# Kernel tuning notes

Hardware: AMD Instinct MI355X
Metric: run time of the kernel (lower is better)

The kernel has to match this reference:

```python
import jax, jax.numpy as jnp
import numpy as np

D_MODEL = 1024
HEADS = 16
D_K = D_MODEL // HEADS
THETA = 10000.0


def _rope(x, pos):
    # x: [B, H, S, d_k]; pos: [S]
    half = D_K // 2
    inv_freq = 1.0 / (THETA ** (jnp.arange(0, D_K, 2, dtype=jnp.float32) / D_K))  # [half]
    ang = pos.astype(jnp.float32)[:, None] * inv_freq[None, :]  # [S, half]
    cos, sin = jnp.cos(ang), jnp.sin(ang)
    x1 = x[..., 0::2]  # even components
    x2 = x[..., 1::2]  # odd components
    o1 = x1 * cos - x2 * sin
    o2 = x1 * sin + x2 * cos
    # interleave back to original layout
    out = jnp.stack([o1, o2], axis=-1).reshape(x.shape)
    return out


def setup_inputs() -> dict:
    key = jax.random.key(0)
    ks = jax.random.split(key, 5)
    B, S = 4, 2048
    scale = 1.0 / np.sqrt(D_MODEL)
    return {
        "x": jax.random.normal(ks[0], (B, S, D_MODEL), dtype=jnp.float32),
        "Wq": jax.random.normal(ks[1], (D_MODEL, D_MODEL), dtype=jnp.float32) * scale,
        "Wk": jax.random.normal(ks[2], (D_MODEL, D_MODEL), dtype=jnp.float32) * scale,
        "Wv": jax.random.normal(ks[3], (D_MODEL, D_MODEL), dtype=jnp.float32) * scale,
        "Wo": jax.random.normal(ks[4], (D_MODEL, D_MODEL), dtype=jnp.float32) * scale,
    }


def reference(x, Wq, Wk, Wv, Wo):
    B, S, _ = x.shape
    # Linear weights are [out, in]; y = x @ W.T
    def proj(W):
        y = jnp.einsum('bsd,ed->bse', x, W)
        return y.reshape(B, S, HEADS, D_K).transpose(0, 2, 1, 3)  # [B,H,S,d_k]
    Q, K, V = proj(Wq), proj(Wk), proj(Wv)
    pos = jnp.arange(S, dtype=jnp.int32)
    Q = _rope(Q, pos)
    K = _rope(K, pos)
    scores = jnp.einsum('bhqd,bhkd->bhqk', Q, K) / jnp.sqrt(jnp.float32(D_K))
    causal = jnp.tril(jnp.ones((S, S), dtype=bool))
    scores = jnp.where(causal, scores, jnp.finfo(scores.dtype).min)
    attn = jax.nn.softmax(scores, axis=-1)
    mh = jnp.einsum('bhqk,bhkd->bhqd', attn, V)  # [B,H,S,d_v]
    mh = mh.transpose(0, 2, 1, 3).reshape(B, S, D_MODEL)
    return jnp.einsum('bsd,ed->bse', mh, Wo)
```

## Files before the change

### kernel.cpp

```cpp
#include <hip/hip_runtime.h>

typedef unsigned short u16;
typedef unsigned int   u32;
typedef __attribute__((ext_vector_type(8))) short s16x8;
typedef __attribute__((ext_vector_type(4))) float f32x4;
typedef __attribute__((ext_vector_type(16))) float f32x16;
typedef __attribute__((ext_vector_type(2))) int i32x2;

#define D_MODEL 1024
#define S_LEN   2048
#define BATCH   4
#define HEADS   16
#define DK      64
#define M_TOTAL (BATCH * S_LEN)

#define QSCALE 0.18033688011112042f
#define ROPE_L2 0.41524101186092029f

__device__ __forceinline__ u16 f2b(float f) {
  u32 u = __float_as_uint(f);
  u32 r = u + 0x7FFFu + ((u >> 16) & 1u);
  return (u16)(r >> 16);
}
__device__ __forceinline__ u32 packtrunc(float f0, float f1) {
  return (__float_as_uint(f0) >> 16) | (__float_as_uint(f1) & 0xFFFF0000u);
}
__device__ __forceinline__ u32 packrn(float f0, float f1) {
  return (u32)f2b(f0) | ((u32)f2b(f1) << 16);
}

extern "C" __device__ float __ocml_native_exp2_f32(float);
__device__ __forceinline__ float fexp2(float x) {
#if __has_builtin(__builtin_amdgcn_exp2f)
  return __builtin_amdgcn_exp2f(x);
#else
  return __ocml_native_exp2_f32(x);
#endif
}

template<int N> __device__ __forceinline__ void waitvm() {
  asm volatile("s_waitcnt vmcnt(%0)" :: "n"(N) : "memory");
}
template<int N> __device__ __forceinline__ void waitlgkm() {
  asm volatile("s_waitcnt lgkmcnt(%0)" :: "n"(N) : "memory");
}

template<int OFF> __device__ __forceinline__ s16x8 ldsr(unsigned a) {
  s16x8 r;
  asm volatile("ds_read_b128 %0, %1 offset:%2" : "=v"(r) : "v"(a), "n"(OFF));
  return r;
}

typedef const __attribute__((address_space(1))) unsigned int* gas_u32p;
typedef __attribute__((address_space(3))) unsigned int* las_u32p;
#define GLL16(gp, lp) __builtin_amdgcn_global_load_lds((gas_u32p)(gp), (las_u32p)(lp), 16, 0, 0)

__global__ void k_cvt(const float* __restrict__ x,
                      const float* __restrict__ a, const float* __restrict__ b,
                      const float* __restrict__ c, const float* __restrict__ d,
                      u16* __restrict__ Xb, u16* __restrict__ Wb) {
  int i = blockIdx.x * blockDim.x + threadIdx.x;
  if (i < 2097152) {
    float4 v = ((const float4*)x)[i];
    ((u32*)Xb)[2 * i]     = packrn(v.x, v.y);
    ((u32*)Xb)[2 * i + 1] = packrn(v.z, v.w);
  } else {
    int j = i - 2097152;
    const float* src = (j < 524288) ? ((j < 262144) ? a : b) : ((j < 786432) ? c : d);
    float4 v = ((const float4*)src)[j & 0x3FFFF];
    ((u32*)Wb)[2 * j]     = packrn(v.x, v.y);
    ((u32*)Wb)[2 * j + 1] = packrn(v.z, v.w);
  }
}

template<bool BF16OUT, bool ROPE, bool DUAL>
__device__ __forceinline__ void gemm_body(u16* __restrict__ SH,
                                          const u16* __restrict__ A, const u16* __restrict__ B,
                                          void* __restrict__ C, void* __restrict__ C2,
                                          int bm, int bn, int N, int K, float scale) {
  constexpr int SLOT = 8192;
  const int tid  = threadIdx.x;
  const int lane = tid & 63;
  const int w    = tid >> 6;
  const int wm2  = w >> 1, wn2 = w & 1;
  const int rl   = lane & 15, q = lane >> 4;

  const int rowS = tid >> 2;
  const int blkS = (tid & 3) ^ ((lane >> 3) & 3);
  const u16* Asrc = A + (size_t)(bm + rowS) * K + blkS * 8;
  const u16* Bsrc = B + (size_t)(bn + rowS) * K + blkS * 8;

  const unsigned shb = (unsigned)(size_t)(las_u32p)SH;
  const int fbase = rl * 32 + ((q ^ ((rl >> 1) & 3)) * 8);
  const unsigned aR0 = shb + 2 * (wm2 * 2048 + fbase);
  const unsigned bR0 = shb + 2 * (4096 + wn2 * 2048 + fbase);

  f32x4 acc[4][4];
#pragma unroll
  for (int i = 0; i < 4; i++)
#pragma unroll
    for (int j = 0; j < 4; j++) acc[i][j] = (f32x4){0.f, 0.f, 0.f, 0.f};

  const int nt = K >> 5;

  auto stage = [&](int t) {
    const int k0 = t << 5;
    u16* d = SH + (t & 1) * SLOT + w * 512;
    GLL16(Asrc + k0, d);
    GLL16(Asrc + (size_t)64 * K + k0, d + 2048);
    GLL16(Bsrc + k0, d + 4096);
    GLL16(Bsrc + (size_t)64 * K + k0, d + 6144);
  };

  stage(0);

  for (int t = 0; t < nt; t++) {
    waitvm<0>();
    __builtin_amdgcn_s_barrier();

    const unsigned off = (unsigned)((t & 1) * (2 * SLOT));
    const unsigned aR = aR0 + off, bR = bR0 + off;
    s16x8 bf0 = ldsr<0>(bR),    bf1 = ldsr<1024>(bR);
    s16x8 bf2 = ldsr<2048>(bR), bf3 = ldsr<3072>(bR);
    s16x8 af0 = ldsr<0>(aR),    af1 = ldsr<1024>(aR);
    s16x8 af2 = ldsr<2048>(aR), af3 = ldsr<3072>(aR);

    if (t + 1 < nt) stage(t + 1);

    waitlgkm<3>();
    __builtin_amdgcn_sched_barrier(0);
    __builtin_amdgcn_s_setprio(1);
    acc[0][0] = __builtin_amdgcn_mfma_f32_16x16x32_bf16(af0, bf0, acc[0][0], 0, 0, 0);
    acc[0][1] = __builtin_amdgcn_mfma_f32_16x16x32_bf16(af0, bf1, acc[0][1], 0, 0, 0);
    acc[0][2] = __builtin_amdgcn_mfma_f32_16x16x32_bf16(af0, bf2, acc[0][2], 0, 0, 0);
    acc[0][3] = __builtin_amdgcn_mfma_f32_16x16x32_bf16(af0, bf3, acc[0][3], 0, 0, 0);
    waitlgkm<2>();
    __builtin_amdgcn_sched_barrier(0);
    acc[1][0] = __builtin_amdgcn_mfma_f32_16x16x32_bf16(af1, bf0, acc[1][0], 0, 0, 0);
    acc[1][1] = __builtin_amdgcn_mfma_f32_16x16x32_bf16(af1, bf1, acc[1][1], 0, 0, 0);
    acc[1][2] = __builtin_amdgcn_mfma_f32_16x16x32_bf16(af1, bf2, acc[1][2], 0, 0, 0);
    acc[1][3] = __builtin_amdgcn_mfma_f32_16x16x32_bf16(af1, bf3, acc[1][3], 0, 0, 0);
    waitlgkm<1>();
    __builtin_amdgcn_sched_barrier(0);
    acc[2][0] = __builtin_amdgcn_mfma_f32_16x16x32_bf16(af2, bf0, acc[2][0], 0, 0, 0);
    acc[2][1] = __builtin_amdgcn_mfma_f32_16x16x32_bf16(af2, bf1, acc[2][1], 0, 0, 0);
    acc[2][2] = __builtin_amdgcn_mfma_f32_16x16x32_bf16(af2, bf2, acc[2][2], 0, 0, 0);
    acc[2][3] = __builtin_amdgcn_mfma_f32_16x16x32_bf16(af2, bf3, acc[2][3], 0, 0, 0);
    waitlgkm<0>();
    __builtin_amdgcn_sched_barrier(0);
    acc[3][0] = __builtin_amdgcn_mfma_f32_16x16x32_bf16(af3, bf0, acc[3][0], 0, 0, 0);
    acc[3][1] = __builtin_amdgcn_mfma_f32_16x16x32_bf16(af3, bf1, acc[3][1], 0, 0, 0);
    acc[3][2] = __builtin_amdgcn_mfma_f32_16x16x32_bf16(af3, bf2, acc[3][2], 0, 0, 0);
    acc[3][3] = __builtin_amdgcn_mfma_f32_16x16x32_bf16(af3, bf3, acc[3][3], 0, 0, 0);
    __builtin_amdgcn_s_setprio(0);
  }

  const bool isQ = !DUAL || (bn < D_MODEL);
  u16* Cd = (u16*)(isQ ? C : C2);
  const int bnL = DUAL ? (bn & (D_MODEL - 1)) : bn;
  const float sc = isQ ? scale : 1.0f;

#pragma unroll
  for (int mi = 0; mi < 4; mi++)
#pragma unroll
    for (int ni = 0; ni < 4; ni++) {
      if (ROPE) {
        const int col = bnL + wn2 * 64 + ni * 16 + rl;
        const int fi  = (col & 63) >> 1;
        const float inv = exp2f(-(float)fi * ROPE_L2);
        const bool odd = (rl & 1);
#pragma unroll
        for (int r = 0; r < 4; r++) {
          int grow = bm + wm2 * 64 + mi * 16 + q * 4 + r;
          float own = acc[mi][ni][r];
          float oth = __shfl_xor(own, 1);
          float ang = (float)(grow & (S_LEN - 1)) * inv;
          float sn, cs;
          __sincosf(ang, &sn, &cs);
          float x1 = odd ? oth : own;
          float x2 = odd ? own : oth;
          float res = odd ? (x1 * sn + x2 * cs) : (x1 * cs - x2 * sn);
          acc[mi][ni][r] = res * sc;
        }
      }
#pragma unroll
      for (int r = 0; r < 4; r++) {
        int grow = bm + wm2 * 64 + mi * 16 + q * 4 + r;
        int gcol = bnL + wn2 * 64 + ni * 16 + rl;
        float v = acc[mi][ni][r];
        if (BF16OUT) Cd[(size_t)grow * N + gcol] = f2b(v);
        else         ((float*)Cd)[(size_t)grow * N + gcol] = v;
      }
    }
}

__launch_bounds__(256, 4)
__global__ void k_qkv(const u16* __restrict__ Xb, const u16* __restrict__ Wqkb,
                      const u16* __restrict__ Wvb,
                      u16* __restrict__ Qb, u16* __restrict__ Kb, u16* __restrict__ Vtg) {
  __shared__ u16 SH[16384];
  const int swz = (blockIdx.x & 7) * 192 + (blockIdx.x >> 3);
  if (swz < 1024) {
    gemm_body<true, true, true>(SH, Xb, Wqkb, Qb, Kb,
                                (swz >> 4) * 128, (swz & 15) * 128,
                                D_MODEL, D_MODEL, QSCALE);
  } else {
    const int b2 = swz - 1024;
    gemm_body<true, false, false>(SH, Wvb, Xb, Vtg, Vtg,
                                  (b2 >> 6) * 128, (b2 & 63) * 128,
                                  M_TOTAL, D_MODEL, 1.0f);
  }
}

__launch_bounds__(256, 4)
__global__ void k_out(const u16* __restrict__ Mh, const u16* __restrict__ Wob,
                      float* __restrict__ out) {
  __shared__ u16 SH[16384];
  const int swz = (blockIdx.x & 7) * 64 + (blockIdx.x >> 3);
  gemm_body<false, false, false>(SH, Mh, Wob, out, out,
                                 (swz >> 3) * 128, (swz & 7) * 128,
                                 D_MODEL, D_MODEL, 1.0f);
}

__launch_bounds__(256, 4)
__global__ void k_attn(const u16* __restrict__ Qb, const u16* __restrict__ Kb,
                       const u16* __restrict__ Vtg, u16* __restrict__ Mh) {
  __shared__ u16 SH[128 * 64 + 64 * 128];
  u16* Kl = SH;
  u16* Vt = SH + 128 * 64;
  const int tid  = threadIdx.x;
  const int lane = tid & 63;
  const int w    = tid >> 6;
  const int n    = lane & 31;
  const int h    = lane >> 5;
  const int nx   = n & 7;
  const int bid = blockIdx.x;
  const int r   = bid >> 3;
  const int u   = r & 15;
  const int bh  = (bid & 7) + 8 * (r >> 4);
  const int hd  = bh & 15, b = bh >> 4;
  const int s   = (w & 2) ? (62 - 2 * u + (w & 1)) : (2 * u + (w & 1));
  const int rb  = s * 32;
  const int ktiles = ((63 - 2 * u) >> 2) + 1;
  const size_t kbase = ((size_t)b * S_LEN) * D_MODEL + (size_t)hd * DK;
  const size_t vbase = ((size_t)hd * DK) * M_TOTAL + (size_t)b * S_LEN;

  const int hx    = ((h ^ nx) << 3);
  const int kidx0 = n * 64  + hx;
  const int vidx0 = n * 128 + hx;

  s16x8 bq[4];
#pragma unroll
  for (int ks = 0; ks < 4; ks++)
    bq[ks] = *(const s16x8*)(Qb + kbase + (size_t)(rb + n) * D_MODEL + ks * 16 + h * 8);

  f32x16 o[2];
#pragma unroll
  for (int dt = 0; dt < 2; dt++)
#pragma unroll
    for (int i = 0; i < 16; i++) o[dt][i] = 0.f;
  float psum = 0.f;

  const int krow_l = lane >> 3;
  const int kblk_l = (lane & 7) ^ krow_l;
  const u16* KgL = Kb + kbase + (size_t)(w * 32 + krow_l) * D_MODEL + kblk_l * 8;
  u16* KdL = Kl + (w * 32) * 64;
  const int vrow_l = lane >> 4;
  const int vblk_l = lane & 15;
  const u16* VgL = Vtg + vbase + (size_t)(w * 16 + vrow_l) * M_TOTAL;
  u16* VdL = Vt + (w * 16) * 128;

  for (int t = 0; t < ktiles; t++) {
    const int k0 = t * 128;
    __syncthreads();
#pragma unroll
    for (int i = 0; i < 4; i++)
      GLL16(KgL + (size_t)(k0 + i * 8) * D_MODEL, KdL + i * 8 * 64);
#pragma unroll
    for (int i = 0; i < 4; i++) {
      const int jj = vblk_l ^ ((i * 4 + vrow_l) & 7);
      GLL16(VgL + (size_t)(i * 4) * M_TOTAL + k0 + jj * 8, VdL + i * 4 * 128);
    }
    __syncthreads();

#pragma unroll
    for (int kt = 0; kt < 4; kt++) {
      const int k0t = k0 + kt * 32;
      if (k0t > rb + 31) continue;

      s16x8 ak[4], vf[4];
#pragma unroll
      for (int ks = 0; ks < 4; ks++)
        ak[ks] = *(const s16x8*)(Kl + ((kidx0 ^ (ks << 4)) + kt * 2048));
#pragma unroll
      for (int c = 0; c < 2; c++)
#pragma unroll
        for (int dt = 0; dt < 2; dt++)
          vf[c * 2 + dt] = *(const s16x8*)(Vt + ((vidx0 ^ (kt * 32 + c * 16)) + dt * 4096));

      f32x16 Sc;
#pragma unroll
      for (int i = 0; i < 16; i++) Sc[i] = 0.f;
#pragma unroll
      for (int ks = 0; ks < 4; ks++)
        Sc = __builtin_amdgcn_mfma_f32_32x32x16_bf16(ak[ks], bq[ks], Sc, 0, 0, 0);

      u32 P0[4], P1[4];
      float ps01 = 0.f, ps23 = 0.f;
      if ((k0t + 31) > rb) {
        const int lim = rb + n - k0t - 4 * h;
#pragma unroll
        for (int g = 0; g < 4; g++) {
          float pv[4];
#pragma unroll
          for (int t2 = 0; t2 < 4; t2++) {
            float e = fexp2(Sc[4 * g + t2]);
            pv[t2] = (8 * g + t2 <= lim) ? e : 0.f;
          }
          ps01 += pv[0] + pv[1];
          ps23 += pv[2] + pv[3];
          P0[g] = packtrunc(pv[0], pv[1]);
          P1[g] = packtrunc(pv[2], pv[3]);
        }
      } else {
#pragma unroll
        for (int g = 0; g < 4; g++) {
          float pv[4];
#pragma unroll
          for (int t2 = 0; t2 < 4; t2++) pv[t2] = fexp2(Sc[4 * g + t2]);
          ps01 += pv[0] + pv[1];
          ps23 += pv[2] + pv[3];
          P0[g] = packtrunc(pv[0], pv[1]);
          P1[g] = packtrunc(pv[2], pv[3]);
        }
      }
      psum += ps01 + ps23;

#pragma unroll
      for (int c = 0; c < 2; c++) {
        i32x2 rA = __builtin_amdgcn_permlane32_swap((int)P0[2 * c], (int)P0[2 * c + 1], false, false);
        i32x2 rB = __builtin_amdgcn_permlane32_swap((int)P1[2 * c], (int)P1[2 * c + 1], false, false);
        union { u32 uu[4]; s16x8 v; } pb;
        pb.uu[0] = (u32)rA[0];
        pb.uu[1] = (u32)rB[0];
        pb.uu[2] = (u32)rA[1];
        pb.uu[3] = (u32)rB[1];
        o[0] = __builtin_amdgcn_mfma_f32_32x32x16_bf16(vf[c * 2 + 0], pb.v, o[0], 0, 0, 0);
        o[1] = __builtin_amdgcn_mfma_f32_32x32x16_bf16(vf[c * 2 + 1], pb.v, o[1], 0, 0, 0);
      }
    }
  }

  float l = psum + __shfl_xor(psum, 32);
  const float linv = 1.0f / l;
  __syncthreads();
  u16* Olw = SH + w * 32 * 66;
#pragma unroll
  for (int dt = 0; dt < 2; dt++) {
#pragma unroll
    for (int g = 0; g < 4; g++) {
      u32 lo = packrn(o[dt][4 * g + 0] * linv, o[dt][4 * g + 1] * linv);
      u32 hi = packrn(o[dt][4 * g + 2] * linv, o[dt][4 * g + 3] * linv);
      *(uint2*)(Olw + n * 66 + dt * 32 + 8 * g + 4 * h) = (uint2){lo, hi};
    }
  }
  const int rr = lane >> 3, seg = lane & 7;
#pragma unroll
  for (int ro = 0; ro < 32; ro += 8) {
    uint4 v = *(const uint4*)(Olw + (ro + rr) * 66 + seg * 8);
    *(uint4*)(Mh + ((size_t)b * S_LEN + rb + ro + rr) * D_MODEL + hd * DK + seg * 8) = v;
  }
}

extern "C" void kernel_launch(void* const* d_in, const int* in_sizes, int n_in,
                              void* d_out, int out_size, void* d_ws, size_t ws_size,
                              hipStream_t stream) {
  const float* x  = (const float*)d_in[0];
  const float* Wq = (const float*)d_in[1];
  const float* Wk = (const float*)d_in[2];
  const float* Wv = (const float*)d_in[3];
  const float* Wo = (const float*)d_in[4];
  float* out = (float*)d_out;

  char* ws = (char*)d_ws;
  const size_t xsz = (size_t)M_TOTAL * D_MODEL * 2;
  const size_t wsz = (size_t)D_MODEL * D_MODEL * 2;
  u16* Xb  = (u16*)ws; ws += xsz;
  u16* Wqb = (u16*)ws; ws += wsz;
  u16* Wkb = (u16*)ws; ws += wsz;
  u16* Wvb = (u16*)ws; ws += wsz;
  u16* Wob = (u16*)ws; ws += wsz;
  u16* Qb  = (u16*)ws; ws += xsz;
  u16* Kb  = (u16*)ws; ws += xsz;
  u16* Vtg = (u16*)ws; ws += xsz;
  u16* Mh  = (u16*)ws; ws += xsz;

  k_cvt<<<12288, 256, 0, stream>>>(x, Wq, Wk, Wv, Wo, Xb, Wqb);

  k_qkv<<<1536, 256, 0, stream>>>(Xb, Wqb, Wvb, Qb, Kb, Vtg);

  k_attn<<<dim3(1024), 256, 0, stream>>>(Qb, Kb, Vtg, Mh);

  k_out<<<512, 256, 0, stream>>>(Mh, Wob, out);
}
```

Measured before the change: 245.2 us.

## Load K and V fragments directly from global memory in attention kernel

Removes the shared-memory staging of K and V tiles and the block-wide barriers; each wave now reads its K and V MFMA fragments straight from global memory (relying on L1/L2) and iterates only over its own causal key tiles. This drops LDS traffic and synchronisation and lets each wave stop at its own diagonal, but it loses cross-wave reuse of the loaded tiles and issues strided, less coalesced global loads with no prefetch overlap.

New measurement: 308.6 us. 1.26x slower.

```diff
diff --git a/kernel.cpp b/kernel.cpp
--- a/kernel.cpp
+++ b/kernel.cpp
@@ -225,15 +225,12 @@
 __launch_bounds__(256, 4)
 __global__ void k_attn(const u16* __restrict__ Qb, const u16* __restrict__ Kb,
                        const u16* __restrict__ Vtg, u16* __restrict__ Mh) {
-  __shared__ u16 SH[128 * 64 + 64 * 128];
-  u16* Kl = SH;
-  u16* Vt = SH + 128 * 64;
+  __shared__ u16 SH[4 * 32 * 66];
   const int tid  = threadIdx.x;
   const int lane = tid & 63;
   const int w    = tid >> 6;
   const int n    = lane & 31;
   const int h    = lane >> 5;
-  const int nx   = n & 7;
   const int bid = blockIdx.x;
   const int r   = bid >> 3;
   const int u   = r & 15;
@@ -241,19 +238,17 @@
   const int hd  = bh & 15, b = bh >> 4;
   const int s   = (w & 2) ? (62 - 2 * u + (w & 1)) : (2 * u + (w & 1));
   const int rb  = s * 32;
-  const int ktiles = ((63 - 2 * u) >> 2) + 1;
   const size_t kbase = ((size_t)b * S_LEN) * D_MODEL + (size_t)hd * DK;
   const size_t vbase = ((size_t)hd * DK) * M_TOTAL + (size_t)b * S_LEN;
 
-  const int hx    = ((h ^ nx) << 3);
-  const int kidx0 = n * 64  + hx;
-  const int vidx0 = n * 128 + hx;
-
   s16x8 bq[4];
 #pragma unroll
   for (int ks = 0; ks < 4; ks++)
     bq[ks] = *(const s16x8*)(Qb + kbase + (size_t)(rb + n) * D_MODEL + ks * 16 + h * 8);
 
+  const u16* KgL = Kb + kbase + (size_t)n * D_MODEL + h * 8;
+  const u16* VgL = Vtg + vbase + (size_t)n * M_TOTAL + h * 8;
+
   f32x16 o[2];
 #pragma unroll
   for (int dt = 0; dt < 2; dt++)
@@ -261,99 +256,73 @@
     for (int i = 0; i < 16; i++) o[dt][i] = 0.f;
   float psum = 0.f;
 
-  const int krow_l = lane >> 3;
-  const int kblk_l = (lane & 7) ^ krow_l;
-  const u16* KgL = Kb + kbase + (size_t)(w * 32 + krow_l) * D_MODEL + kblk_l * 8;
-  u16* KdL = Kl + (w * 32) * 64;
-  const int vrow_l = lane >> 4;
-  const int vblk_l = lane & 15;
-  const u16* VgL = Vtg + vbase + (size_t)(w * 16 + vrow_l) * M_TOTAL;
-  u16* VdL = Vt + (w * 16) * 128;
-
-  for (int t = 0; t < ktiles; t++) {
-    const int k0 = t * 128;
-    __syncthreads();
-#pragma unroll
-    for (int i = 0; i < 4; i++)
-      GLL16(KgL + (size_t)(k0 + i * 8) * D_MODEL, KdL + i * 8 * 64);
-#pragma unroll
-    for (int i = 0; i < 4; i++) {
-      const int jj = vblk_l ^ ((i * 4 + vrow_l) & 7);
-      GLL16(VgL + (size_t)(i * 4) * M_TOTAL + k0 + jj * 8, VdL + i * 4 * 128);
-    }
-    __syncthreads();
-
-#pragma unroll
-    for (int kt = 0; kt < 4; kt++) {
-      const int k0t = k0 + kt * 32;
-      if (k0t > rb + 31) continue;
-
-      s16x8 ak[4], vf[4];
-#pragma unroll
-      for (int ks = 0; ks < 4; ks++)
-        ak[ks] = *(const s16x8*)(Kl + ((kidx0 ^ (ks << 4)) + kt * 2048));
-#pragma unroll
-      for (int c = 0; c < 2; c++)
-#pragma unroll
-        for (int dt = 0; dt < 2; dt++)
-          vf[c * 2 + dt] = *(const s16x8*)(Vt + ((vidx0 ^ (kt * 32 + c * 16)) + dt * 4096));
-
-      f32x16 Sc;
-#pragma unroll
-      for (int i = 0; i < 16; i++) Sc[i] = 0.f;
-#pragma unroll
-      for (int ks = 0; ks < 4; ks++)
-        Sc = __builtin_amdgcn_mfma_f32_32x32x16_bf16(ak[ks], bq[ks], Sc, 0, 0, 0);
-
-      u32 P0[4], P1[4];
-      float ps01 = 0.f, ps23 = 0.f;
-      if ((k0t + 31) > rb) {
-        const int lim = rb + n - k0t - 4 * h;
-#pragma unroll
-        for (int g = 0; g < 4; g++) {
-          float pv[4];
-#pragma unroll
-          for (int t2 = 0; t2 < 4; t2++) {
-            float e = fexp2(Sc[4 * g + t2]);
-            pv[t2] = (8 * g + t2 <= lim) ? e : 0.f;
-          }
-          ps01 += pv[0] + pv[1];
-          ps23 += pv[2] + pv[3];
-          P0[g] = packtrunc(pv[0], pv[1]);
-          P1[g] = packtrunc(pv[2], pv[3]);
+  for (int st = 0; st <= s; st++) {
+    const int k0t = st * 32;
+
+    s16x8 ak[4], vf[4];
+#pragma unroll
+    for (int ks = 0; ks < 4; ks++)
+      ak[ks] = *(const s16x8*)(KgL + (size_t)k0t * D_MODEL + ks * 16);
+#pragma unroll
+    for (int c = 0; c < 2; c++)
+#pragma unroll
+      for (int dt = 0; dt < 2; dt++)
+        vf[c * 2 + dt] = *(const s16x8*)(VgL + (size_t)(dt * 32) * M_TOTAL + k0t + c * 16);
+
+    f32x16 Sc;
+#pragma unroll
+    for (int i = 0; i < 16; i++) Sc[i] = 0.f;
+#pragma unroll
+    for (int ks = 0; ks < 4; ks++)
+      Sc = __builtin_amdgcn_mfma_f32_32x32x16_bf16(ak[ks], bq[ks], Sc, 0, 0, 0);
+
+    u32 P0[4], P1[4];
+    float ps01 = 0.f, ps23 = 0.f;
+    if (st == s) {
+      const int lim = rb + n - k0t - 4 * h;
+#pragma unroll
+      for (int g = 0; g < 4; g++) {
+        float pv[4];
+#pragma unroll
+        for (int t2 = 0; t2 < 4; t2++) {
+          float e = fexp2(Sc[4 * g + t2]);
+          pv[t2] = (8 * g + t2 <= lim) ? e : 0.f;
         }
-      } else {
-#pragma unroll
-        for (int g = 0; g < 4; g++) {
-          float pv[4];
-#pragma unroll
-          for (int t2 = 0; t2 < 4; t2++) pv[t2] = fexp2(Sc[4 * g + t2]);
-          ps01 += pv[0] + pv[1];
-          ps23 += pv[2] + pv[3];
-          P0[g] = packtrunc(pv[0], pv[1]);
-          P1[g] = packtrunc(pv[2], pv[3]);
-        }
+        ps01 += pv[0] + pv[1];
+        ps23 += pv[2] + pv[3];
+        P0[g] = packtrunc(pv[0], pv[1]);
+        P1[g] = packtrunc(pv[2], pv[3]);
       }
-      psum += ps01 + ps23;
-
-#pragma unroll
-      for (int c = 0; c < 2; c++) {
-        i32x2 rA = __builtin_amdgcn_permlane32_swap((int)P0[2 * c], (int)P0[2 * c + 1], false, false);
-        i32x2 rB = __builtin_amdgcn_permlane32_swap((int)P1[2 * c], (int)P1[2 * c + 1], false, false);
-        union { u32 uu[4]; s16x8 v; } pb;
-        pb.uu[0] = (u32)rA[0];
-        pb.uu[1] = (u32)rB[0];
-        pb.uu[2] = (u32)rA[1];
-        pb.uu[3] = (u32)rB[1];
-        o[0] = __builtin_amdgcn_mfma_f32_32x32x16_bf16(vf[c * 2 + 0], pb.v, o[0], 0, 0, 0);
-        o[1] = __builtin_amdgcn_mfma_f32_32x32x16_bf16(vf[c * 2 + 1], pb.v, o[1], 0, 0, 0);
+    } else {
+#pragma unroll
+      for (int g = 0; g < 4; g++) {
+        float pv[4];
+#pragma unroll
+        for (int t2 = 0; t2 < 4; t2++) pv[t2] = fexp2(Sc[4 * g + t2]);
+        ps01 += pv[0] + pv[1];
+        ps23 += pv[2] + pv[3];
+        P0[g] = packtrunc(pv[0], pv[1]);
+        P1[g] = packtrunc(pv[2], pv[3]);
       }
     }
+    psum += ps01 + ps23;
+
+#pragma unroll
+    for (int c = 0; c < 2; c++) {
+      i32x2 rA = __builtin_amdgcn_permlane32_swap((int)P0[2 * c], (int)P0[2 * c + 1], false, false);
+      i32x2 rB = __builtin_amdgcn_permlane32_swap((int)P1[2 * c], (int)P1[2 * c + 1], false, false);
+      union { u32 uu[4]; s16x8 v; } pb;
+      pb.uu[0] = (u32)rA[0];
+      pb.uu[1] = (u32)rB[0];
+      pb.uu[2] = (u32)rA[1];
+      pb.uu[3] = (u32)rB[1];
+      o[0] = __builtin_amdgcn_mfma_f32_32x32x16_bf16(vf[c * 2 + 0], pb.v, o[0], 0, 0, 0);
+      o[1] = __builtin_amdgcn_mfma_f32_32x32x16_bf16(vf[c * 2 + 1], pb.v, o[1], 0, 0, 0);
+    }
   }
 
   float l = psum + __shfl_xor(psum, 32);
   const float linv = 1.0f / l;
-  __syncthreads();
   u16* Olw = SH + w * 32 * 66;
 #pragma unroll
   for (int dt = 0; dt < 2; dt++) {
```
